# Optimization experiments

Measured on AMD Instinct MI355X. Metric: run time of the kernel, lower is better.

The kernel has to match this reference:

```python
import jax, jax.numpy as jnp
import numpy as np

B, S, NX, H = 8, 1024, 1024, 16
D = NX // H  # head_features = 64
SCALE = True


def setup_inputs() -> dict:
    key = jax.random.key(0)
    k1, k2, k3 = jax.random.split(key, 3)
    x = jax.random.normal(k1, (B, S, NX), dtype=jnp.float32)
    w_attn = jax.random.normal(k2, (NX, 3 * NX), dtype=jnp.float32) * 0.02
    b_attn = jnp.zeros((3 * NX,), dtype=jnp.float32)
    w_proj = jax.random.normal(k3, (NX, NX), dtype=jnp.float32) * 0.02
    b_proj = jnp.zeros((NX,), dtype=jnp.float32)
    return {"x": x, "w_attn": w_attn, "b_attn": b_attn, "w_proj": w_proj, "b_proj": b_proj}


def _split_heads(t):
    # (B, S, NX) -> (B, H, S, D)
    return t.reshape(B, S, H, D).transpose(0, 2, 1, 3)


def reference(x, w_attn, b_attn, w_proj, b_proj):
    # fused QKV projection (Conv1D): addmm over flattened tokens
    qkv = x @ w_attn + b_attn                      # (B, S, 3*NX)
    q, k, v = jnp.split(qkv, 3, axis=-1)
    q = _split_heads(q)                            # (B, H, S, D)
    k = _split_heads(k)
    v = _split_heads(v)

    w = jnp.einsum("bhqd,bhkd->bhqk", q, k)        # full S x S scores
    if SCALE:
        w = w / jnp.sqrt(jnp.asarray(D, w.dtype))
    # causal mask applied exactly as in the source: multiply + big-negative subtract
    b = jnp.tril(jnp.ones((S, S), dtype=w.dtype))[None, None]
    w = w * b - 1e10 * (1.0 - b)
    w = jax.nn.softmax(w, axis=-1)                 # attn_pdrop = 0 (eval)
    a = jnp.einsum("bhqk,bhkd->bhqd", w, v)        # (B, H, S, D)

    # merge heads: (B, H, S, D) -> (B, S, NX)
    a = a.transpose(0, 2, 1, 3).reshape(B, S, NX)
    a = a @ w_proj + b_proj                        # c_proj; resid_pdrop = 0 (eval)
    return a
```

## Files before the change

kernel.cpp:

```cpp
#include <hip/hip_runtime.h>
#include <hip/hip_bf16.h>

#define BB 8
#define SS 1024
#define NXX 1024
#define HH 16
#define DD 64
#define MM (BB * SS)

typedef __attribute__((ext_vector_type(8))) short short8;
typedef __attribute__((ext_vector_type(4))) short short4v;
typedef __attribute__((ext_vector_type(4))) float float4v;

static __device__ inline short bf16bits(float v) {
    __hip_bfloat16 t = __float2bfloat16(v);
    return *reinterpret_cast<short*>(&t);
}

__global__ __launch_bounds__(256) void prep_kernel(
    const float* __restrict__ x, __hip_bfloat16* __restrict__ xb,
    const float* __restrict__ w_attn, __hip_bfloat16* __restrict__ wT_attn,
    const float* __restrict__ w_proj, __hip_bfloat16* __restrict__ wT_proj)
{
    __shared__ __hip_bfloat16 tile[32][33];
    const int blk = blockIdx.x;
    const int tid = threadIdx.x;

    if (blk < 8192) {
        int i = blk * 1024 + tid * 4;
        float4 v = *(const float4*)(x + i);
        xb[i + 0] = __float2bfloat16(v.x);
        xb[i + 1] = __float2bfloat16(v.y);
        xb[i + 2] = __float2bfloat16(v.z);
        xb[i + 3] = __float2bfloat16(v.w);
        return;
    }
    const float* W;
    __hip_bfloat16* Wt;
    int K, N, idx;
    if (blk < 8192 + 3072) { idx = blk - 8192;  W = w_attn; Wt = wT_attn; K = NXX; N = 3 * NXX; }
    else                   { idx = blk - 11264; W = w_proj; Wt = wT_proj; K = NXX; N = NXX; }
    const int k0 = (idx % (K / 32)) * 32;
    const int n0 = (idx / (K / 32)) * 32;
    const int tx = tid % 32;
    const int ty = tid / 32;
#pragma unroll
    for (int p = 0; p < 4; ++p) {
        int k = ty + p * 8;
        tile[k][tx] = __float2bfloat16(W[(size_t)(k0 + k) * N + n0 + tx]);
    }
    __syncthreads();
#pragma unroll
    for (int p = 0; p < 4; ++p) {
        int nn = ty + p * 8;
        Wt[(size_t)(n0 + nn) * K + k0 + tx] = tile[tx][nn];
    }
}

#define STAGE_A(DST, kk)                                                       \
    {                                                                          \
        _Pragma("unroll") for (int j_ = 0; j_ < 2; ++j_) {                     \
            const __hip_bfloat16* s_ = aSrc + (size_t)(j_ * 128) * K + (kk);   \
            char* d_ = (char*)(DST) + j_ * 8192 + (wave << 10);                \
            __builtin_amdgcn_global_load_lds(                                  \
                (const __attribute__((address_space(1))) void*)s_,             \
                (__attribute__((address_space(3))) void*)d_, 16, 0, 0);        \
        }                                                                      \
    }

#define STAGE_B(DST, kk)                                                       \
    {                                                                          \
        const __hip_bfloat16* s_ = bSrc + (kk);                                \
        char* d_ = (char*)(DST) + (wave << 10);                                \
        __builtin_amdgcn_global_load_lds(                                      \
            (const __attribute__((address_space(1))) void*)s_,                 \
            (__attribute__((address_space(3))) void*)d_, 16, 0, 0);            \
    }

#define WAIT_LGKM0_FENCED()                                                    \
    asm volatile("s_waitcnt lgkmcnt(0)" ::: "memory");                         \
    __builtin_amdgcn_sched_barrier(0);

template <int MODE>
__global__ __launch_bounds__(512, 2) void gemm256(
    const __hip_bfloat16* __restrict__ A,
    const __hip_bfloat16* __restrict__ Bt,
    const float* __restrict__ bias,
    void* __restrict__ Cv,
    __hip_bfloat16* __restrict__ vT,
    int M, int K, int N)
{
    __shared__ __attribute__((aligned(16))) char smem[65536];

    const int tid  = threadIdx.x;
    const int wave = tid >> 6;
    const int lane = tid & 63;
    const int wm = (wave >> 1) << 6;
    const int wn = (wave & 1) << 6;

    const int nwg = (int)gridDim.x;
    const int cpx = nwg >> 3;
    const int bid = (int)blockIdx.x;
    const int swz = (bid & 7) * cpx + (bid >> 3);
    const int ntN = N >> 7;
    const int width = ntN << 3;
    const int group = swz / width;
    const int w = swz % width;
    const int m0 = ((group << 3) + (w & 7)) << 8;
    const int n0 = (w >> 3) << 7;

    const int NT = K >> 5;

    const int row_s  = tid >> 2;
    const int srccol = (((tid & 3) ^ ((tid >> 3) & 3)) << 3);
    const __hip_bfloat16* aSrc = A  + (size_t)(m0 + row_s) * K + srccol;
    const __hip_bfloat16* bSrc = Bt + (size_t)(n0 + row_s) * K + srccol;

    const int l15 = lane & 15, q4 = lane >> 4;
    const int sslot = (q4 ^ ((l15 >> 1) & 3)) << 4;
    const int offA = (wm + l15) * 64 + sslot;
    const int offB = (wn + l15) * 64 + sslot;

    float4v acc[4][4];
#pragma unroll
    for (int i = 0; i < 4; ++i)
#pragma unroll
        for (int j = 0; j < 4; ++j) acc[i][j] = (float4v){0.f, 0.f, 0.f, 0.f};

    char* const Abuf0 = (char*)smem;
    char* const Bbuf0 = (char*)smem + 49152;

    STAGE_A(Abuf0,          0);
    STAGE_B(Bbuf0,          0);
    STAGE_A(Abuf0 + 16384, 32);
    STAGE_B(Bbuf0 +  8192, 32);
    asm volatile("s_waitcnt vmcnt(3)" ::: "memory");
    __builtin_amdgcn_s_barrier();

    int ia = 0;
    for (int t = 0; t < NT; ++t) {
        const char* Ab = Abuf0 + ia * 16384;
        char* Bb = Bbuf0 + ((t & 1) << 13);
        const int ia2 = (ia == 0) ? 2 : ia - 1;

        short8 a[4], b[4];

#pragma unroll
        for (int mf = 0; mf < 2; ++mf) a[mf] = *(const short8*)(Ab + offA + mf * 1024);
#pragma unroll
        for (int nf = 0; nf < 4; ++nf) b[nf] = *(const short8*)(Bb + offB + nf * 1024);
        if (t + 2 < NT) STAGE_A(Abuf0 + ia2 * 16384, (t + 2) << 5);
        __builtin_amdgcn_s_barrier();
        WAIT_LGKM0_FENCED();
        __builtin_amdgcn_s_setprio(1);
#pragma unroll
        for (int mf = 0; mf < 2; ++mf)
#pragma unroll
            for (int nf = 0; nf < 4; ++nf)
                acc[mf][nf] = __builtin_amdgcn_mfma_f32_16x16x32_bf16(
                    a[mf], b[nf], acc[mf][nf], 0, 0, 0);
        __builtin_amdgcn_s_setprio(0);
        __builtin_amdgcn_s_barrier();

#pragma unroll
        for (int mf = 2; mf < 4; ++mf) a[mf] = *(const short8*)(Ab + offA + mf * 1024);
        if (t + 2 < NT) {
            STAGE_B(Bb, (t + 2) << 5);
            asm volatile("s_waitcnt vmcnt(3)" ::: "memory");
        } else if (t + 1 < NT) {
            asm volatile("s_waitcnt vmcnt(0)" ::: "memory");
        }
        __builtin_amdgcn_s_barrier();
        WAIT_LGKM0_FENCED();
        __builtin_amdgcn_s_setprio(1);
#pragma unroll
        for (int mf = 2; mf < 4; ++mf)
#pragma unroll
            for (int nf = 0; nf < 4; ++nf)
                acc[mf][nf] = __builtin_amdgcn_mfma_f32_16x16x32_bf16(
                    a[mf], b[nf], acc[mf][nf], 0, 0, 0);
        __builtin_amdgcn_s_setprio(0);
        __builtin_amdgcn_s_barrier();

        ia = (ia == 2) ? 0 : ia + 1;
    }

    const int cr = q4 * 4;
    const int cc = l15;

    if (MODE == 1 && n0 >= 2048) {
        const int bb = m0 / SS;
#pragma unroll
        for (int mf = 0; mf < 4; ++mf) {
            int grow = m0 + wm + mf * 16 + cr;
            int ssr = grow & (SS - 1);
#pragma unroll
            for (int nf = 0; nf < 4; ++nf) {
                int gcol = n0 + wn + nf * 16 + cc;
                float bv = bias[gcol];
                int col = gcol - 2048;
                int hh = col >> 6, dd = col & 63;
                short4v pk;
#pragma unroll
                for (int r = 0; r < 4; ++r) pk[r] = bf16bits(acc[mf][nf][r] + bv);
                *(short4v*)(vT + (size_t)((bb * HH + hh) * 64 + dd) * SS + ssr) = pk;
            }
        }
    } else {
        const float qs = (MODE == 1 && n0 < 1024) ? 0.125f : 1.0f;
#pragma unroll
        for (int mf = 0; mf < 4; ++mf) {
            int grow = m0 + wm + mf * 16 + cr;
#pragma unroll
            for (int nf = 0; nf < 4; ++nf) {
                int gcol = n0 + wn + nf * 16 + cc;
                float bv = bias[gcol];
#pragma unroll
                for (int r = 0; r < 4; ++r) {
                    float v = (acc[mf][nf][r] + bv) * qs;
                    if constexpr (MODE == 1)
                        ((__hip_bfloat16*)Cv)[(size_t)(grow + r) * N + gcol] =
                            __float2bfloat16(v);
                    else
                        ((float*)Cv)[(size_t)(grow + r) * N + gcol] = v;
                }
            }
        }
    }
}

#define PSTR 72

__global__ __launch_bounds__(256) void attn_mfma_kernel(
    const __hip_bfloat16* __restrict__ qkv,
    const __hip_bfloat16* __restrict__ vT,
    __hip_bfloat16* __restrict__ aout)
{
    const int bh = blockIdx.x;
    const int b = bh / HH, h = bh % HH;
    const int q0 = ((int)gridDim.y - 1 - (int)blockIdx.y) * 128;

    __shared__ __hip_bfloat16 Ks[64 * PSTR];
    __shared__ __hip_bfloat16 Vs[64 * PSTR];
    __shared__ __hip_bfloat16 Ps[4][32 * PSTR];

    const int tid  = threadIdx.x;
    const int wave = tid >> 6;
    const int lane = tid & 63;
    const int quad = lane >> 4;
    const int l16  = lane & 15;

    short8 qf[2][2];
#pragma unroll
    for (int t = 0; t < 2; ++t) {
        const __hip_bfloat16* qp = qkv +
            (size_t)(b * SS + q0 + wave * 32 + t * 16 + l16) * 3072 + h * 64 + quad * 8;
        qf[t][0] = *(const short8*)qp;
        qf[t][1] = *(const short8*)(qp + 32);
    }

    float4v o_acc[2][4];
    float l_acc[2][4];
#pragma unroll
    for (int t = 0; t < 2; ++t)
#pragma unroll
        for (int nt = 0; nt < 4; ++nt) o_acc[t][nt] = (float4v){0.f, 0.f, 0.f, 0.f};
#pragma unroll
    for (int t = 0; t < 2; ++t)
#pragma unroll
        for (int r = 0; r < 4; ++r) l_acc[t][r] = 0.f;

    const int sk  = tid & 63;
    const int sdo = (tid >> 6) * 16;
    const int vd  = tid >> 2;
    const int vko = (tid & 3) * 16;
    const int qmin_w = q0 + wave * 32;
    const int nkt = q0 / 64 + 2;

    for (int kt = 0; kt < nkt; ++kt) {
        const int k0 = kt * 64;
        __syncthreads();
        {
            const __hip_bfloat16* kr =
                qkv + (size_t)(b * SS + k0 + sk) * 3072 + 1024 + h * 64 + sdo;
            *(short8*)&Ks[sk * PSTR + sdo]     = *(const short8*)kr;
            *(short8*)&Ks[sk * PSTR + sdo + 8] = *(const short8*)(kr + 8);
            const __hip_bfloat16* vr = vT + (size_t)(bh * 64 + vd) * SS + k0 + vko;
            *(short8*)&Vs[vd * PSTR + vko]     = *(const short8*)vr;
            *(short8*)&Vs[vd * PSTR + vko + 8] = *(const short8*)(vr + 8);
        }
        __syncthreads();
        if (k0 > qmin_w + 31) continue;

        const short* ks = (const short*)Ks;
        float4v sacc[2][4];
#pragma unroll
        for (int t = 0; t < 2; ++t)
#pragma unroll
            for (int nt = 0; nt < 4; ++nt) sacc[t][nt] = (float4v){0.f, 0.f, 0.f, 0.f};
#pragma unroll
        for (int kc = 0; kc < 2; ++kc)
#pragma unroll
            for (int nt = 0; nt < 4; ++nt) {
                short8 kb = *(const short8*)(ks + (nt * 16 + l16) * PSTR + kc * 32 + quad * 8);
                sacc[0][nt] = __builtin_amdgcn_mfma_f32_16x16x32_bf16(qf[0][kc], kb, sacc[0][nt], 0, 0, 0);
                sacc[1][nt] = __builtin_amdgcn_mfma_f32_16x16x32_bf16(qf[1][kc], kb, sacc[1][nt], 0, 0, 0);
            }

        const bool needmask = (k0 + 63 > qmin_w);
        __hip_bfloat16* pw = Ps[wave];
#pragma unroll
        for (int t = 0; t < 2; ++t)
#pragma unroll
            for (int nt = 0; nt < 4; ++nt) {
                int kk = k0 + nt * 16 + l16;
#pragma unroll
                for (int r = 0; r < 4; ++r) {
                    float s = sacc[t][nt][r];
                    if (needmask) {
                        int qq = qmin_w + t * 16 + quad * 4 + r;
                        if (kk > qq) s = -1e10f;
                    }
                    float p = __expf(s);
                    l_acc[t][r] += p;
                    pw[(t * 16 + quad * 4 + r) * PSTR + nt * 16 + l16] =
                        __float2bfloat16(p);
                }
            }

        const short* ps = (const short*)pw;
        const short* vs = (const short*)Vs;
#pragma unroll
        for (int kc = 0; kc < 2; ++kc) {
            short8 pa0 = *(const short8*)(ps + (0 * 16 + l16) * PSTR + kc * 32 + quad * 8);
            short8 pa1 = *(const short8*)(ps + (1 * 16 + l16) * PSTR + kc * 32 + quad * 8);
#pragma unroll
            for (int nt = 0; nt < 4; ++nt) {
                short8 vb = *(const short8*)(vs + (nt * 16 + l16) * PSTR + kc * 32 + quad * 8);
                o_acc[0][nt] = __builtin_amdgcn_mfma_f32_16x16x32_bf16(pa0, vb, o_acc[0][nt], 0, 0, 0);
                o_acc[1][nt] = __builtin_amdgcn_mfma_f32_16x16x32_bf16(pa1, vb, o_acc[1][nt], 0, 0, 0);
            }
        }
    }

#pragma unroll
    for (int t = 0; t < 2; ++t)
#pragma unroll
        for (int r = 0; r < 4; ++r) {
            float l = l_acc[t][r];
            l += __shfl_xor(l, 1);
            l += __shfl_xor(l, 2);
            l += __shfl_xor(l, 4);
            l += __shfl_xor(l, 8);
            float inv = 1.f / l;
            int row = q0 + wave * 32 + t * 16 + quad * 4 + r;
            __hip_bfloat16* op = aout + (size_t)(b * SS + row) * NXX + h * 64 + l16;
#pragma unroll
            for (int nt = 0; nt < 4; ++nt)
                op[nt * 16] = __float2bfloat16(o_acc[t][nt][r] * inv);
        }
}

extern "C" void kernel_launch(void* const* d_in, const int* in_sizes, int n_in,
                              void* d_out, int out_size, void* d_ws, size_t ws_size,
                              hipStream_t stream)
{
    const float* x      = (const float*)d_in[0];
    const float* w_attn = (const float*)d_in[1];
    const float* b_attn = (const float*)d_in[2];
    const float* w_proj = (const float*)d_in[3];
    const float* b_proj = (const float*)d_in[4];
    float* out = (float*)d_out;

    char* ws = (char*)d_ws;
    __hip_bfloat16* qkv     = (__hip_bfloat16*)ws;
    __hip_bfloat16* vT      = (__hip_bfloat16*)(ws + (size_t)48 * 1024 * 1024);
    __hip_bfloat16* xb      = (__hip_bfloat16*)(ws + (size_t)64 * 1024 * 1024);
    __hip_bfloat16* amid    = xb;
    __hip_bfloat16* wT_attn = (__hip_bfloat16*)(ws + (size_t)80 * 1024 * 1024);
    __hip_bfloat16* wT_proj = (__hip_bfloat16*)(ws + (size_t)86 * 1024 * 1024);

    prep_kernel<<<dim3(12288), dim3(256), 0, stream>>>(
        x, xb, w_attn, wT_attn, w_proj, wT_proj);

    gemm256<1><<<dim3((MM / 256) * ((3 * NXX) / 128)), dim3(512), 0, stream>>>(
        xb, wT_attn, b_attn, qkv, vT, MM, NXX, 3 * NXX);

    attn_mfma_kernel<<<dim3(BB * HH, SS / 128), dim3(256), 0, stream>>>(qkv, vT, amid);

    gemm256<0><<<dim3((MM / 256) * (NXX / 128)), dim3(512), 0, stream>>>(
        amid, wT_proj, b_proj, out, nullptr, MM, NXX, NXX);
}
```

Baseline: 215.5 us.

## Enlarge GEMM tile to 256x256 with double-buffered A and B staging

After: 236.4 us. 1.1x slower.

```diff
diff --git a/kernel.cpp b/kernel.cpp
--- a/kernel.cpp
+++ b/kernel.cpp
@@ -57,24 +57,15 @@
     }
 }
 
-#define STAGE_A(DST, kk)                                                       \
+#define STAGE(SRCBASE, DST, kk)                                                \
     {                                                                          \
         _Pragma("unroll") for (int j_ = 0; j_ < 2; ++j_) {                     \
-            const __hip_bfloat16* s_ = aSrc + (size_t)(j_ * 128) * K + (kk);   \
+            const __hip_bfloat16* s_ = (SRCBASE) + (size_t)(j_ * 128) * K + (kk); \
             char* d_ = (char*)(DST) + j_ * 8192 + (wave << 10);                \
             __builtin_amdgcn_global_load_lds(                                  \
                 (const __attribute__((address_space(1))) void*)s_,             \
                 (__attribute__((address_space(3))) void*)d_, 16, 0, 0);        \
         }                                                                      \
-    }
-
-#define STAGE_B(DST, kk)                                                       \
-    {                                                                          \
-        const __hip_bfloat16* s_ = bSrc + (kk);                                \
-        char* d_ = (char*)(DST) + (wave << 10);                                \
-        __builtin_amdgcn_global_load_lds(                                      \
-            (const __attribute__((address_space(1))) void*)s_,                 \
-            (__attribute__((address_space(3))) void*)d_, 16, 0, 0);            \
     }
 
 #define WAIT_LGKM0_FENCED()                                                    \
@@ -96,18 +87,18 @@
     const int wave = tid >> 6;
     const int lane = tid & 63;
     const int wm = (wave >> 1) << 6;
-    const int wn = (wave & 1) << 6;
+    const int wn = (wave & 1) << 7;
 
     const int nwg = (int)gridDim.x;
     const int cpx = nwg >> 3;
     const int bid = (int)blockIdx.x;
     const int swz = (bid & 7) * cpx + (bid >> 3);
-    const int ntN = N >> 7;
+    const int ntN = N >> 8;
     const int width = ntN << 3;
     const int group = swz / width;
     const int w = swz % width;
     const int m0 = ((group << 3) + (w & 7)) << 8;
-    const int n0 = (w >> 3) << 7;
+    const int n0 = (w >> 3) << 8;
 
     const int NT = K >> 5;
 
@@ -121,40 +112,37 @@
     const int offA = (wm + l15) * 64 + sslot;
     const int offB = (wn + l15) * 64 + sslot;
 
-    float4v acc[4][4];
+    float4v acc[4][8];
 #pragma unroll
     for (int i = 0; i < 4; ++i)
 #pragma unroll
-        for (int j = 0; j < 4; ++j) acc[i][j] = (float4v){0.f, 0.f, 0.f, 0.f};
-
-    char* const Abuf0 = (char*)smem;
-    char* const Bbuf0 = (char*)smem + 49152;
-
-    STAGE_A(Abuf0,          0);
-    STAGE_B(Bbuf0,          0);
-    STAGE_A(Abuf0 + 16384, 32);
-    STAGE_B(Bbuf0 +  8192, 32);
-    asm volatile("s_waitcnt vmcnt(3)" ::: "memory");
+        for (int j = 0; j < 8; ++j) acc[i][j] = (float4v){0.f, 0.f, 0.f, 0.f};
+
+    char* const A0 = (char*)smem;
+    char* const B0 = (char*)smem + 32768;
+
+    STAGE(aSrc, A0,          0);
+    STAGE(bSrc, B0,          0);
+    STAGE(aSrc, A0 + 16384, 32);
+    asm volatile("s_waitcnt vmcnt(2)" ::: "memory");
     __builtin_amdgcn_s_barrier();
 
-    int ia = 0;
     for (int t = 0; t < NT; ++t) {
-        const char* Ab = Abuf0 + ia * 16384;
-        char* Bb = Bbuf0 + ((t & 1) << 13);
-        const int ia2 = (ia == 0) ? 2 : ia - 1;
-
-        short8 a[4], b[4];
-
-#pragma unroll
-        for (int mf = 0; mf < 2; ++mf) a[mf] = *(const short8*)(Ab + offA + mf * 1024);
+        const char* Ab = A0 + ((t & 1) << 14);
+        const char* Bb = B0 + ((t & 1) << 14);
+
+        short8 a[4], b[8];
+
+#pragma unroll
+        for (int mf = 0; mf < 4; ++mf) a[mf] = *(const short8*)(Ab + offA + mf * 1024);
 #pragma unroll
         for (int nf = 0; nf < 4; ++nf) b[nf] = *(const short8*)(Bb + offB + nf * 1024);
-        if (t + 2 < NT) STAGE_A(Abuf0 + ia2 * 16384, (t + 2) << 5);
+        if (t + 1 < NT) STAGE(bSrc, B0 + (((t + 1) & 1) << 14), (t + 1) << 5);
         __builtin_amdgcn_s_barrier();
         WAIT_LGKM0_FENCED();
         __builtin_amdgcn_s_setprio(1);
 #pragma unroll
-        for (int mf = 0; mf < 2; ++mf)
+        for (int mf = 0; mf < 4; ++mf)
 #pragma unroll
             for (int nf = 0; nf < 4; ++nf)
                 acc[mf][nf] = __builtin_amdgcn_mfma_f32_16x16x32_bf16(
@@ -163,10 +151,10 @@
         __builtin_amdgcn_s_barrier();
 
 #pragma unroll
-        for (int mf = 2; mf < 4; ++mf) a[mf] = *(const short8*)(Ab + offA + mf * 1024);
+        for (int nf = 4; nf < 8; ++nf) b[nf] = *(const short8*)(Bb + offB + nf * 1024);
         if (t + 2 < NT) {
-            STAGE_B(Bb, (t + 2) << 5);
-            asm volatile("s_waitcnt vmcnt(3)" ::: "memory");
+            STAGE(aSrc, A0 + ((t & 1) << 14), (t + 2) << 5);
+            asm volatile("s_waitcnt vmcnt(2)" ::: "memory");
         } else if (t + 1 < NT) {
             asm volatile("s_waitcnt vmcnt(0)" ::: "memory");
         }
@@ -174,15 +162,13 @@
         WAIT_LGKM0_FENCED();
         __builtin_amdgcn_s_setprio(1);
 #pragma unroll
-        for (int mf = 2; mf < 4; ++mf)
-#pragma unroll
-            for (int nf = 0; nf < 4; ++nf)
+        for (int mf = 0; mf < 4; ++mf)
+#pragma unroll
+            for (int nf = 4; nf < 8; ++nf)
                 acc[mf][nf] = __builtin_amdgcn_mfma_f32_16x16x32_bf16(
                     a[mf], b[nf], acc[mf][nf], 0, 0, 0);
         __builtin_amdgcn_s_setprio(0);
         __builtin_amdgcn_s_barrier();
-
-        ia = (ia == 2) ? 0 : ia + 1;
     }
 
     const int cr = q4 * 4;
@@ -195,7 +181,7 @@
             int grow = m0 + wm + mf * 16 + cr;
             int ssr = grow & (SS - 1);
 #pragma unroll
-            for (int nf = 0; nf < 4; ++nf) {
+            for (int nf = 0; nf < 8; ++nf) {
                 int gcol = n0 + wn + nf * 16 + cc;
                 float bv = bias[gcol];
                 int col = gcol - 2048;
@@ -212,7 +198,7 @@
         for (int mf = 0; mf < 4; ++mf) {
             int grow = m0 + wm + mf * 16 + cr;
 #pragma unroll
-            for (int nf = 0; nf < 4; ++nf) {
+            for (int nf = 0; nf < 8; ++nf) {
                 int gcol = n0 + wn + nf * 16 + cc;
                 float bv = bias[gcol];
 #pragma unroll
@@ -383,11 +369,11 @@
     prep_kernel<<<dim3(12288), dim3(256), 0, stream>>>(
         x, xb, w_attn, wT_attn, w_proj, wT_proj);
 
-    gemm256<1><<<dim3((MM / 256) * ((3 * NXX) / 128)), dim3(512), 0, stream>>>(
+    gemm256<1><<<dim3((MM / 256) * ((3 * NXX) / 256)), dim3(512), 0, stream>>>(
         xb, wT_attn, b_attn, qkv, vT, MM, NXX, 3 * NXX);
 
     attn_mfma_kernel<<<dim3(BB * HH, SS / 128), dim3(256), 0, stream>>>(qkv, vT, amid);
 
-    gemm256<0><<<dim3((MM / 256) * (NXX / 128)), dim3(512), 0, stream>>>(
+    gemm256<0><<<dim3((MM / 256) * (NXX / 256)), dim3(512), 0, stream>>>(
         amid, wT_proj, b_proj, out, nullptr, MM, NXX, NXX);
 }
```

## Pair causal query blocks per workgroup and register-prefetch next K/V tile

Applied to the files above, without the earlier changes.

After: 223.8 us. 1.04x slower.

```diff
diff --git a/kernel.cpp b/kernel.cpp
--- a/kernel.cpp
+++ b/kernel.cpp
@@ -238,7 +238,7 @@
 {
     const int bh = blockIdx.x;
     const int b = bh / HH, h = bh % HH;
-    const int q0 = ((int)gridDim.y - 1 - (int)blockIdx.y) * 128;
+    const int qb = blockIdx.y;
 
     __shared__ __hip_bfloat16 Ks[64 * PSTR];
     __shared__ __hip_bfloat16 Vs[64 * PSTR];
@@ -250,115 +250,135 @@
     const int quad = lane >> 4;
     const int l16  = lane & 15;
 
-    short8 qf[2][2];
-#pragma unroll
-    for (int t = 0; t < 2; ++t) {
-        const __hip_bfloat16* qp = qkv +
-            (size_t)(b * SS + q0 + wave * 32 + t * 16 + l16) * 3072 + h * 64 + quad * 8;
-        qf[t][0] = *(const short8*)qp;
-        qf[t][1] = *(const short8*)(qp + 32);
-    }
-
-    float4v o_acc[2][4];
-    float l_acc[2][4];
-#pragma unroll
-    for (int t = 0; t < 2; ++t)
-#pragma unroll
-        for (int nt = 0; nt < 4; ++nt) o_acc[t][nt] = (float4v){0.f, 0.f, 0.f, 0.f};
-#pragma unroll
-    for (int t = 0; t < 2; ++t)
-#pragma unroll
-        for (int r = 0; r < 4; ++r) l_acc[t][r] = 0.f;
-
     const int sk  = tid & 63;
     const int sdo = (tid >> 6) * 16;
     const int vd  = tid >> 2;
     const int vko = (tid & 3) * 16;
-    const int qmin_w = q0 + wave * 32;
-    const int nkt = q0 / 64 + 2;
-
-    for (int kt = 0; kt < nkt; ++kt) {
-        const int k0 = kt * 64;
-        __syncthreads();
+
+    for (int pass = 0; pass < 2; ++pass) {
+        const int q0 = (pass == 0 ? qb : 7 - qb) * 128;
+        const int qmin_w = q0 + wave * 32;
+        const int nkt = q0 / 64 + 2;
+
+        short8 qf[2][2];
+#pragma unroll
+        for (int t = 0; t < 2; ++t) {
+            const __hip_bfloat16* qp = qkv +
+                (size_t)(b * SS + q0 + wave * 32 + t * 16 + l16) * 3072 + h * 64 + quad * 8;
+            qf[t][0] = *(const short8*)qp;
+            qf[t][1] = *(const short8*)(qp + 32);
+        }
+
+        float4v o_acc[2][4];
+        float l_acc[2][4];
+#pragma unroll
+        for (int t = 0; t < 2; ++t)
+#pragma unroll
+            for (int nt = 0; nt < 4; ++nt) o_acc[t][nt] = (float4v){0.f, 0.f, 0.f, 0.f};
+#pragma unroll
+        for (int t = 0; t < 2; ++t)
+#pragma unroll
+            for (int r = 0; r < 4; ++r) l_acc[t][r] = 0.f;
+
+        short8 kreg0, kreg1, vreg0, vreg1;
         {
             const __hip_bfloat16* kr =
-                qkv + (size_t)(b * SS + k0 + sk) * 3072 + 1024 + h * 64 + sdo;
-            *(short8*)&Ks[sk * PSTR + sdo]     = *(const short8*)kr;
-            *(short8*)&Ks[sk * PSTR + sdo + 8] = *(const short8*)(kr + 8);
-            const __hip_bfloat16* vr = vT + (size_t)(bh * 64 + vd) * SS + k0 + vko;
-            *(short8*)&Vs[vd * PSTR + vko]     = *(const short8*)vr;
-            *(short8*)&Vs[vd * PSTR + vko + 8] = *(const short8*)(vr + 8);
-        }
-        __syncthreads();
-        if (k0 > qmin_w + 31) continue;
-
-        const short* ks = (const short*)Ks;
-        float4v sacc[2][4];
-#pragma unroll
-        for (int t = 0; t < 2; ++t)
-#pragma unroll
-            for (int nt = 0; nt < 4; ++nt) sacc[t][nt] = (float4v){0.f, 0.f, 0.f, 0.f};
-#pragma unroll
-        for (int kc = 0; kc < 2; ++kc)
-#pragma unroll
-            for (int nt = 0; nt < 4; ++nt) {
-                short8 kb = *(const short8*)(ks + (nt * 16 + l16) * PSTR + kc * 32 + quad * 8);
-                sacc[0][nt] = __builtin_amdgcn_mfma_f32_16x16x32_bf16(qf[0][kc], kb, sacc[0][nt], 0, 0, 0);
-                sacc[1][nt] = __builtin_amdgcn_mfma_f32_16x16x32_bf16(qf[1][kc], kb, sacc[1][nt], 0, 0, 0);
+                qkv + (size_t)(b * SS + sk) * 3072 + 1024 + h * 64 + sdo;
+            kreg0 = *(const short8*)kr;
+            kreg1 = *(const short8*)(kr + 8);
+            const __hip_bfloat16* vr = vT + (size_t)(bh * 64 + vd) * SS + vko;
+            vreg0 = *(const short8*)vr;
+            vreg1 = *(const short8*)(vr + 8);
+        }
+
+        for (int kt = 0; kt < nkt; ++kt) {
+            const int k0 = kt * 64;
+            __syncthreads();
+            *(short8*)&Ks[sk * PSTR + sdo]     = kreg0;
+            *(short8*)&Ks[sk * PSTR + sdo + 8] = kreg1;
+            *(short8*)&Vs[vd * PSTR + vko]     = vreg0;
+            *(short8*)&Vs[vd * PSTR + vko + 8] = vreg1;
+            __syncthreads();
+            if (kt + 1 < nkt) {
+                const int k1 = k0 + 64;
+                const __hip_bfloat16* kr =
+                    qkv + (size_t)(b * SS + k1 + sk) * 3072 + 1024 + h * 64 + sdo;
+                kreg0 = *(const short8*)kr;
+                kreg1 = *(const short8*)(kr + 8);
+                const __hip_bfloat16* vr = vT + (size_t)(bh * 64 + vd) * SS + k1 + vko;
+                vreg0 = *(const short8*)vr;
+                vreg1 = *(const short8*)(vr + 8);
             }
-
-        const bool needmask = (k0 + 63 > qmin_w);
-        __hip_bfloat16* pw = Ps[wave];
-#pragma unroll
-        for (int t = 0; t < 2; ++t)
-#pragma unroll
-            for (int nt = 0; nt < 4; ++nt) {
-                int kk = k0 + nt * 16 + l16;
-#pragma unroll
-                for (int r = 0; r < 4; ++r) {
-                    float s = sacc[t][nt][r];
-                    if (needmask) {
-                        int qq = qmin_w + t * 16 + quad * 4 + r;
-                        if (kk > qq) s = -1e10f;
+            if (k0 > qmin_w + 31) continue;
+
+            const short* ks = (const short*)Ks;
+            float4v sacc[2][4];
+#pragma unroll
+            for (int t = 0; t < 2; ++t)
+#pragma unroll
+                for (int nt = 0; nt < 4; ++nt) sacc[t][nt] = (float4v){0.f, 0.f, 0.f, 0.f};
+#pragma unroll
+            for (int kc = 0; kc < 2; ++kc)
+#pragma unroll
+                for (int nt = 0; nt < 4; ++nt) {
+                    short8 kb = *(const short8*)(ks + (nt * 16 + l16) * PSTR + kc * 32 + quad * 8);
+                    sacc[0][nt] = __builtin_amdgcn_mfma_f32_16x16x32_bf16(qf[0][kc], kb, sacc[0][nt], 0, 0, 0);
+                    sacc[1][nt] = __builtin_amdgcn_mfma_f32_16x16x32_bf16(qf[1][kc], kb, sacc[1][nt], 0, 0, 0);
+                }
+
+            const bool needmask = (k0 + 63 > qmin_w);
+            __hip_bfloat16* pw = Ps[wave];
+#pragma unroll
+            for (int t = 0; t < 2; ++t)
+#pragma unroll
+                for (int nt = 0; nt < 4; ++nt) {
+                    int kk = k0 + nt * 16 + l16;
+#pragma unroll
+                    for (int r = 0; r < 4; ++r) {
+                        float s = sacc[t][nt][r];
+                        if (needmask) {
+                            int qq = qmin_w + t * 16 + quad * 4 + r;
+                            if (kk > qq) s = -1e10f;
+                        }
+                        float p = __expf(s);
+                        l_acc[t][r] += p;
+                        pw[(t * 16 + quad * 4 + r) * PSTR + nt * 16 + l16] =
+                            __float2bfloat16(p);
                     }
-                    float p = __expf(s);
-                    l_acc[t][r] += p;
-                    pw[(t * 16 + quad * 4 + r) * PSTR + nt * 16 + l16] =
-                        __float2bfloat16(p);
+                }
+
+            const short* ps = (const short*)pw;
+            const short* vs = (const short*)Vs;
+#pragma unroll
+            for (int kc = 0; kc < 2; ++kc) {
+                short8 pa0 = *(const short8*)(ps + (0 * 16 + l16) * PSTR + kc * 32 + quad * 8);
+                short8 pa1 = *(const short8*)(ps + (1 * 16 + l16) * PSTR + kc * 32 + quad * 8);
+#pragma unroll
+                for (int nt = 0; nt < 4; ++nt) {
+                    short8 vb = *(const short8*)(vs + (nt * 16 + l16) * PSTR + kc * 32 + quad * 8);
+                    o_acc[0][nt] = __builtin_amdgcn_mfma_f32_16x16x32_bf16(pa0, vb, o_acc[0][nt], 0, 0, 0);
+                    o_acc[1][nt] = __builtin_amdgcn_mfma_f32_16x16x32_bf16(pa1, vb, o_acc[1][nt], 0, 0, 0);
                 }
             }
-
-        const short* ps = (const short*)pw;
-        const short* vs = (const short*)Vs;
-#pragma unroll
-        for (int kc = 0; kc < 2; ++kc) {
-            short8 pa0 = *(const short8*)(ps + (0 * 16 + l16) * PSTR + kc * 32 + quad * 8);
-            short8 pa1 = *(const short8*)(ps + (1 * 16 + l16) * PSTR + kc * 32 + quad * 8);
-#pragma unroll
-            for (int nt = 0; nt < 4; ++nt) {
-                short8 vb = *(const short8*)(vs + (nt * 16 + l16) * PSTR + kc * 32 + quad * 8);
-                o_acc[0][nt] = __builtin_amdgcn_mfma_f32_16x16x32_bf16(pa0, vb, o_acc[0][nt], 0, 0, 0);
-                o_acc[1][nt] = __builtin_amdgcn_mfma_f32_16x16x32_bf16(pa1, vb, o_acc[1][nt], 0, 0, 0);
+        }
+
+#pragma unroll
+        for (int t = 0; t < 2; ++t)
+#pragma unroll
+            for (int r = 0; r < 4; ++r) {
+                float l = l_acc[t][r];
+                l += __shfl_xor(l, 1);
+                l += __shfl_xor(l, 2);
+                l += __shfl_xor(l, 4);
+                l += __shfl_xor(l, 8);
+                float inv = 1.f / l;
+                int row = q0 + wave * 32 + t * 16 + quad * 4 + r;
+                __hip_bfloat16* op = aout + (size_t)(b * SS + row) * NXX + h * 64 + l16;
+#pragma unroll
+                for (int nt = 0; nt < 4; ++nt)
+                    op[nt * 16] = __float2bfloat16(o_acc[t][nt][r] * inv);
             }
-        }
-    }
-
-#pragma unroll
-    for (int t = 0; t < 2; ++t)
-#pragma unroll
-        for (int r = 0; r < 4; ++r) {
-            float l = l_acc[t][r];
-            l += __shfl_xor(l, 1);
-            l += __shfl_xor(l, 2);
-            l += __shfl_xor(l, 4);
-            l += __shfl_xor(l, 8);
-            float inv = 1.f / l;
-            int row = q0 + wave * 32 + t * 16 + quad * 4 + r;
-            __hip_bfloat16* op = aout + (size_t)(b * SS + row) * NXX + h * 64 + l16;
-#pragma unroll
-            for (int nt = 0; nt < 4; ++nt)
-                op[nt * 16] = __float2bfloat16(o_acc[t][nt][r] * inv);
-        }
+    }
 }
 
 extern "C" void kernel_launch(void* const* d_in, const int* in_sizes, int n_in,
@@ -386,7 +406,7 @@
     gemm256<1><<<dim3((MM / 256) * ((3 * NXX) / 128)), dim3(512), 0, stream>>>(
         xb, wT_attn, b_attn, qkv, vT, MM, NXX, 3 * NXX);
 
-    attn_mfma_kernel<<<dim3(BB * HH, SS / 128), dim3(256), 0, stream>>>(qkv, vT, amid);
+    attn_mfma_kernel<<<dim3(BB * HH, 4), dim3(256), 0, stream>>>(qkv, vT, amid);
 
     gemm256<0><<<dim3((MM / 256) * (NXX / 128)), dim3(512), 0, stream>>>(
         amid, wT_proj, b_proj, out, nullptr, MM, NXX, NXX);
```
